# Kernel optimization log

Measured on AMD Instinct MI355X. Metric: run time of the kernel, lower is better.

The kernel has to match this reference:

```python
import jax, jax.numpy as jnp
import numpy as np

SEQ_LEN = 2_097_152  # free sequence dimension
NUM_SYMBOLS = 10
NUM_STATES = 10
NUM_CLASSES = 2


def setup_inputs() -> dict:
    key = jax.random.key(0)
    k1, k2, k3, k4 = jax.random.split(key, 4)
    # x[t] is a probability distribution over symbols (soft one-hot), matching
    # the automaton semantics and keeping the 2M-step recurrence numerically stable.
    x = jax.random.uniform(k1, (SEQ_LEN, NUM_SYMBOLS), dtype=jnp.float32)
    x = x / jnp.sum(x, axis=1, keepdims=True)
    # Parameters, initialized exactly as in the torch module (__init__ softmaxes).
    P = jax.nn.softmax(jax.random.normal(k2, (NUM_SYMBOLS, NUM_STATES, NUM_STATES), dtype=jnp.float32), axis=2)
    start_state = jax.nn.softmax(jax.random.normal(k3, (NUM_STATES,), dtype=jnp.float32), axis=0)
    accept_states = jax.nn.softmax(jax.random.normal(k4, (NUM_STATES, NUM_CLASSES), dtype=jnp.float32), axis=1)
    return {"x": x, "P": P, "start_state": start_state, "accept_states": accept_states}


def reference(x, P, start_state, accept_states):
    # Sequential recurrence: s_{t+1} = s_t @ (sum_k x[t,k] * P[k])
    def step(s, xt):
        Wt = jnp.einsum('k,kij->ij', xt, P)  # [S, S] symbol-weighted transition
        return s @ Wt, None
    s, _ = jax.lax.scan(step, start_state, x)
    return s @ accept_states  # [num_classes]
```

## Files before the change

### kernel.cpp

```cpp
#include <hip/hip_runtime.h>

#define TEN 10

typedef float v2f __attribute__((ext_vector_type(2)));

__global__ __attribute__((amdgpu_flat_work_group_size(256, 256),
                          amdgpu_waves_per_eu(1, 1)))
void automaton_chunks(const float* __restrict__ x, const float* __restrict__ P,
                      float* __restrict__ outBlk, long long T, int C)
{
    __shared__ __align__(16) float lds[8704];

    const int tid  = threadIdx.x;
    const int wave = tid >> 6;
    const int lane = tid & 63;
    const int grp  = lane / 5;
    const int sub  = lane % 5;
    const bool active = (grp < 12);
    const int cib  = wave * 12 + grp;
    const int j0 = 2 * sub, j1 = j0 + 1;

    v2f p2[TEN][TEN];
    v2f m2[2][5];
    long long Lc = 0;
    const float2* xp = nullptr;
    float* slot = lds + (active ? cib : 0) * 132;

    if (active) {
        const long long chunk = (long long)blockIdx.x * 48 + cib;
        const long long s0 = chunk * T / C;
        const long long s1 = (chunk + 1) * T / C;
        Lc = s1 - s0;
        xp = reinterpret_cast<const float2*>(x) + s0 * 5;
#pragma unroll
        for (int k = 0; k < TEN; ++k)
#pragma unroll
            for (int a = 0; a < TEN; ++a) {
                const float2 v = *reinterpret_cast<const float2*>(P + k * 100 + a * TEN + j0);
                p2[k][a].x = v.x;
                p2[k][a].y = v.y;
            }
#pragma unroll
        for (int c = 0; c < 2; ++c)
#pragma unroll
            for (int i = 0; i < 5; ++i) {
                const int jc = 2 * sub + c;
                m2[c][i].x = (2 * i     == jc) ? 1.0f : 0.0f;
                m2[c][i].y = (2 * i + 1 == jc) ? 1.0f : 0.0f;
            }
    }

    float2 nx0, nx1, nx2, nx3, nx4;
    if (active) { nx0 = xp[0]; nx1 = xp[1]; nx2 = xp[2]; nx3 = xp[3]; nx4 = xp[4]; xp += 5; }

    if (active) {
#pragma unroll 1
        for (long long s = 0; s < Lc; ++s) {
            const float xs[TEN] = {nx0.x, nx0.y, nx1.x, nx1.y, nx2.x,
                                   nx2.y, nx3.x, nx3.y, nx4.x, nx4.y};
            v2f xv2[TEN];
#pragma unroll
            for (int k = 0; k < TEN; ++k) { xv2[k].x = xs[k]; xv2[k].y = xs[k]; }
            if (s + 1 < Lc) {
                nx0 = xp[0]; nx1 = xp[1]; nx2 = xp[2]; nx3 = xp[3]; nx4 = xp[4];
                xp += 5;
            }

            {
                float* c0 = slot + j0 * 12;
                reinterpret_cast<float4*>(c0)[0] = make_float4(m2[0][0].x, m2[0][0].y, m2[0][1].x, m2[0][1].y);
                reinterpret_cast<float4*>(c0)[1] = make_float4(m2[0][2].x, m2[0][2].y, m2[0][3].x, m2[0][3].y);
                reinterpret_cast<float2*>(c0 + 8)[0] = make_float2(m2[0][4].x, m2[0][4].y);
                float* c1 = slot + j1 * 12;
                reinterpret_cast<float4*>(c1)[0] = make_float4(m2[1][0].x, m2[1][0].y, m2[1][1].x, m2[1][1].y);
                reinterpret_cast<float4*>(c1)[1] = make_float4(m2[1][2].x, m2[1][2].y, m2[1][3].x, m2[1][3].y);
                reinterpret_cast<float2*>(c1 + 8)[0] = make_float2(m2[1][4].x, m2[1][4].y);
            }
            __builtin_amdgcn_wave_barrier();

            v2f w2[TEN];
#pragma unroll
            for (int a = 0; a < TEN; ++a) {
                v2f acc = xv2[0] * p2[0][a];
#pragma unroll
                for (int k = 1; k < TEN; ++k)
                    acc = __builtin_elementwise_fma(xv2[k], p2[k][a], acc);
                w2[a] = acc;
            }

#pragma unroll
            for (int a = 0; a < TEN; ++a) {
                const float4 v0 = reinterpret_cast<const float4*>(slot + a * 12)[0];
                const float4 v1 = reinterpret_cast<const float4*>(slot + a * 12)[1];
                const float2 v2 = reinterpret_cast<const float2*>(slot + a * 12 + 8)[0];
                v2f cc[5];
                cc[0].x = v0.x; cc[0].y = v0.y;
                cc[1].x = v0.z; cc[1].y = v0.w;
                cc[2].x = v1.x; cc[2].y = v1.y;
                cc[3].x = v1.z; cc[3].y = v1.w;
                cc[4].x = v2.x; cc[4].y = v2.y;
                v2f wb0, wb1;
                wb0.x = w2[a].x; wb0.y = w2[a].x;
                wb1.x = w2[a].y; wb1.y = w2[a].y;
                if (a == 0) {
#pragma unroll
                    for (int i = 0; i < 5; ++i) {
                        m2[0][i] = cc[i] * wb0;
                        m2[1][i] = cc[i] * wb1;
                    }
                } else {
#pragma unroll
                    for (int i = 0; i < 5; ++i) {
                        m2[0][i] = __builtin_elementwise_fma(cc[i], wb0, m2[0][i]);
                        m2[1][i] = __builtin_elementwise_fma(cc[i], wb1, m2[1][i]);
                    }
                }
            }
            __builtin_amdgcn_wave_barrier();
        }
    }

    __syncthreads();
    if (active) {
        float* t = lds + cib * 120;
#pragma unroll
        for (int i = 0; i < 5; ++i) {
            t[(2 * i)     * 12 + j0] = m2[0][i].x;
            t[(2 * i + 1) * 12 + j0] = m2[0][i].y;
            t[(2 * i)     * 12 + j1] = m2[1][i].x;
            t[(2 * i + 1) * 12 + j1] = m2[1][i].y;
        }
    }
    __syncthreads();

    {
        const float* src = lds;
        float* dst = lds + 5760;
        int n = 48;
        while (n > 3) {
            const int np = n >> 1;
            const int pI = tid / TEN;
            const int r  = tid % TEN;
            if (pI < np) {
                const float* A = src + (2 * pI) * 120;
                const float* B = src + (2 * pI + 1) * 120;
                float ar[TEN];
#pragma unroll
                for (int j = 0; j < TEN; ++j) ar[j] = A[r * 12 + j];
                float c[TEN] = {0, 0, 0, 0, 0, 0, 0, 0, 0, 0};
#pragma unroll
                for (int a = 0; a < TEN; ++a) {
                    const float ma = ar[a];
#pragma unroll
                    for (int j = 0; j < TEN; ++j) c[j] = fmaf(ma, B[a * 12 + j], c[j]);
                }
                float* Cp = dst + pI * 120;
#pragma unroll
                for (int j = 0; j < TEN; ++j) Cp[r * 12 + j] = c[j];
            }
            __syncthreads();
            const float* ts = src; src = dst; dst = const_cast<float*>(ts);
            n = np;
        }
        if (tid < TEN) {
            const int r = tid;
            float ar[TEN];
#pragma unroll
            for (int j = 0; j < TEN; ++j) ar[j] = src[r * 12 + j];
            float c[TEN] = {0, 0, 0, 0, 0, 0, 0, 0, 0, 0};
#pragma unroll
            for (int a = 0; a < TEN; ++a) {
                const float ma = ar[a];
#pragma unroll
                for (int j = 0; j < TEN; ++j) c[j] = fmaf(ma, src[120 + a * 12 + j], c[j]);
            }
#pragma unroll
            for (int j = 0; j < TEN; ++j) lds[5760 + r * 12 + j] = c[j];
        }
        __syncthreads();
        if (tid < TEN) {
            const int r = tid;
            float c[TEN] = {0, 0, 0, 0, 0, 0, 0, 0, 0, 0};
#pragma unroll
            for (int a = 0; a < TEN; ++a) {
                const float ma = lds[5760 + r * 12 + a];
#pragma unroll
                for (int j = 0; j < TEN; ++j) c[j] = fmaf(ma, src[240 + a * 12 + j], c[j]);
            }
            float* dr = outBlk + (size_t)blockIdx.x * 100 + r * TEN;
#pragma unroll
            for (int j = 0; j < TEN; ++j) dr[j] = c[j];
        }
    }
}

__device__ __forceinline__ void tree64(float* lds, int tid)
{
    const int q     = tid >> 2;
    const int sub   = tid & 3;
    const int rbase = (sub == 3) ? 8 : sub * 3;
    const int r0 = rbase, r1 = rbase + 1;
    const int r2 = (rbase + 2 > 9) ? 9 : rbase + 2;
    const bool w2 = (sub < 2);

    for (int np = 32; np >= 1; np >>= 1) {
        float c[3][TEN];
        if (q < np) {
            const float* A = lds + (2 * q) * 120;
            const float* B = lds + (2 * q + 1) * 120;
            float ar[3][TEN];
#pragma unroll
            for (int t = 0; t < 3; ++t) {
                const int rt = (t == 0) ? r0 : (t == 1) ? r1 : r2;
                const float4 a0 = reinterpret_cast<const float4*>(A + rt * 12)[0];
                const float4 a1 = reinterpret_cast<const float4*>(A + rt * 12)[1];
                const float2 a2 = reinterpret_cast<const float2*>(A + rt * 12 + 8)[0];
                ar[t][0]=a0.x; ar[t][1]=a0.y; ar[t][2]=a0.z; ar[t][3]=a0.w;
                ar[t][4]=a1.x; ar[t][5]=a1.y; ar[t][6]=a1.z; ar[t][7]=a1.w;
                ar[t][8]=a2.x; ar[t][9]=a2.y;
#pragma unroll
                for (int j = 0; j < TEN; ++j) c[t][j] = 0.0f;
            }
#pragma unroll
            for (int a = 0; a < TEN; ++a) {
                const float4 b0 = reinterpret_cast<const float4*>(B + a * 12)[0];
                const float4 b1 = reinterpret_cast<const float4*>(B + a * 12)[1];
                const float2 b2 = reinterpret_cast<const float2*>(B + a * 12 + 8)[0];
                const float br[TEN] = {b0.x,b0.y,b0.z,b0.w,b1.x,b1.y,b1.z,b1.w,b2.x,b2.y};
#pragma unroll
                for (int t = 0; t < 3; ++t) {
                    const float ma = ar[t][a];
#pragma unroll
                    for (int j = 0; j < TEN; ++j) c[t][j] = fmaf(ma, br[j], c[t][j]);
                }
            }
        }
        __syncthreads();
        if (q < np) {
            float* C = lds + q * 120;
#pragma unroll
            for (int t = 0; t < 3; ++t) {
                const int rt = (t == 0) ? r0 : (t == 1) ? r1 : r2;
                if (t < 2 || w2) {
                    float* cr = C + rt * 12;
                    reinterpret_cast<float4*>(cr)[0] = make_float4(c[t][0], c[t][1], c[t][2], c[t][3]);
                    reinterpret_cast<float4*>(cr)[1] = make_float4(c[t][4], c[t][5], c[t][6], c[t][7]);
                    reinterpret_cast<float2*>(cr + 8)[0] = make_float2(c[t][8], c[t][9]);
                }
            }
        }
        __syncthreads();
    }
}

__global__ void automaton_final(const float* __restrict__ blkM,
                                const float* __restrict__ start,
                                const float* __restrict__ acc,
                                float* __restrict__ outv)
{
    __shared__ __align__(16) float lds[7680];
    __shared__ float sv[TEN];
    const int tid = threadIdx.x;
    const int q   = tid >> 2;
    const int sub = tid & 3;
    const int rbase = (sub == 3) ? 8 : sub * 3;
    const int rr0 = rbase, rr1 = rbase + 1;
    const int rr2 = (rbase + 2 > 9) ? 9 : rbase + 2;
    const bool w2 = (sub < 2);

    float a[3][TEN];
    {
        const int rr[3] = {rr0, rr1, rr2};
        const float* A0 = blkM + (size_t)(4 * q) * 100;
#pragma unroll
        for (int t = 0; t < 3; ++t) {
            const float2* pp = reinterpret_cast<const float2*>(A0 + rr[t] * TEN);
            const float2 a0 = pp[0], a1 = pp[1], a2 = pp[2], a3 = pp[3], a4 = pp[4];
            a[t][0]=a0.x; a[t][1]=a0.y; a[t][2]=a1.x; a[t][3]=a1.y; a[t][4]=a2.x;
            a[t][5]=a2.y; a[t][6]=a3.x; a[t][7]=a3.y; a[t][8]=a4.x; a[t][9]=a4.y;
        }
    }
#pragma unroll 1
    for (int i = 1; i < 4; ++i) {
        const float* B = blkM + (size_t)(4 * q + i) * 100;
        float c[3][TEN];
#pragma unroll
        for (int t = 0; t < 3; ++t)
#pragma unroll
            for (int j = 0; j < TEN; ++j) c[t][j] = 0.0f;
#pragma unroll
        for (int aa = 0; aa < TEN; ++aa) {
            const float2* br = reinterpret_cast<const float2*>(B + aa * TEN);
            const float2 b0 = br[0], b1 = br[1], b2 = br[2], b3 = br[3], b4 = br[4];
            const float bv[TEN] = {b0.x,b0.y,b1.x,b1.y,b2.x,b2.y,b3.x,b3.y,b4.x,b4.y};
#pragma unroll
            for (int t = 0; t < 3; ++t) {
                const float ma = a[t][aa];
#pragma unroll
                for (int j = 0; j < TEN; ++j) c[t][j] = fmaf(ma, bv[j], c[t][j]);
            }
        }
#pragma unroll
        for (int t = 0; t < 3; ++t)
#pragma unroll
            for (int j = 0; j < TEN; ++j) a[t][j] = c[t][j];
    }
    {
        float* dst = lds + q * 120;
#pragma unroll
        for (int t = 0; t < 3; ++t) {
            const int rt = (t == 0) ? rr0 : (t == 1) ? rr1 : rr2;
            if (t < 2 || w2) {
                float* dr = dst + rt * 12;
                reinterpret_cast<float4*>(dr)[0] = make_float4(a[t][0], a[t][1], a[t][2], a[t][3]);
                reinterpret_cast<float4*>(dr)[1] = make_float4(a[t][4], a[t][5], a[t][6], a[t][7]);
                reinterpret_cast<float2*>(dr + 8)[0] = make_float2(a[t][8], a[t][9]);
            }
        }
    }
    __syncthreads();
    tree64(lds, tid);

    if (tid < TEN) {
        const int j = tid;
        float v = 0.0f;
#pragma unroll
        for (int r = 0; r < TEN; ++r) v = fmaf(start[r], lds[r * 12 + j], v);
        sv[j] = v;
    }
    __syncthreads();
    if (tid == 0) {
        float o0 = 0.0f, o1 = 0.0f;
#pragma unroll
        for (int j = 0; j < TEN; ++j) {
            o0 = fmaf(sv[j], acc[2 * j + 0], o0);
            o1 = fmaf(sv[j], acc[2 * j + 1], o1);
        }
        outv[0] = o0;
        outv[1] = o1;
    }
}

extern "C" void kernel_launch(void* const* d_in, const int* in_sizes, int n_in,
                              void* d_out, int out_size, void* d_ws, size_t ws_size,
                              hipStream_t stream)
{
    const float* x     = (const float*)d_in[0];
    const float* P     = (const float*)d_in[1];
    const float* start = (const float*)d_in[2];
    const float* acc   = (const float*)d_in[3];
    float* out         = (float*)d_out;

    const long long T = (long long)in_sizes[0] / TEN;
    const int C = 12288;

    float* blkM = (float*)d_ws;

    automaton_chunks<<<256, 256, 0, stream>>>(x, P, blkM, T, C);
    automaton_final<<<1, 256, 0, stream>>>(blkM, start, acc, out);
}
```

Measured before the change: 267.7 us.

## Double chunk count, allow two waves per EU, use op_sel packed FMA asm

```diff
diff --git a/kernel.cpp b/kernel.cpp
--- a/kernel.cpp
+++ b/kernel.cpp
@@ -4,8 +4,16 @@
 
 typedef float v2f __attribute__((ext_vector_type(2)));
 
+#define PK_MUL_S0LO(d,s0,s1)   asm("v_pk_mul_f32 %0, %1, %2 op_sel:[0,0] op_sel_hi:[0,1]"         : "=v"(d)  : "v"(s0), "v"(s1))
+#define PK_FMA_S0LO(acc,s0,s1) asm("v_pk_fma_f32 %0, %1, %2, %0 op_sel:[0,0,0] op_sel_hi:[0,1,1]" : "+v"(acc) : "v"(s0), "v"(s1))
+#define PK_FMA_S0HI(acc,s0,s1) asm("v_pk_fma_f32 %0, %1, %2, %0 op_sel:[1,0,0] op_sel_hi:[1,1,1]" : "+v"(acc) : "v"(s0), "v"(s1))
+#define PK_MUL_S1LO(d,s0,s1)   asm("v_pk_mul_f32 %0, %1, %2 op_sel:[0,0] op_sel_hi:[1,0]"         : "=v"(d)  : "v"(s0), "v"(s1))
+#define PK_MUL_S1HI(d,s0,s1)   asm("v_pk_mul_f32 %0, %1, %2 op_sel:[0,1] op_sel_hi:[1,1]"         : "=v"(d)  : "v"(s0), "v"(s1))
+#define PK_FMA_S1LO(acc,s0,s1) asm("v_pk_fma_f32 %0, %1, %2, %0 op_sel:[0,0,0] op_sel_hi:[1,0,1]" : "+v"(acc) : "v"(s0), "v"(s1))
+#define PK_FMA_S1HI(acc,s0,s1) asm("v_pk_fma_f32 %0, %1, %2, %0 op_sel:[0,1,0] op_sel_hi:[1,1,1]" : "+v"(acc) : "v"(s0), "v"(s1))
+
 __global__ __attribute__((amdgpu_flat_work_group_size(256, 256),
-                          amdgpu_waves_per_eu(1, 1)))
+                          amdgpu_waves_per_eu(2, 2)))
 void automaton_chunks(const float* __restrict__ x, const float* __restrict__ P,
                       float* __restrict__ outBlk, long long T, int C)
 {
@@ -22,16 +30,17 @@
 
     v2f p2[TEN][TEN];
     v2f m2[2][5];
-    long long Lc = 0;
-    const float2* xp = nullptr;
+    int Lc = 0;
+    const v2f* xp = nullptr;
     float* slot = lds + (active ? cib : 0) * 132;
+    float* wb0  = slot + j0 * 12;
 
     if (active) {
         const long long chunk = (long long)blockIdx.x * 48 + cib;
         const long long s0 = chunk * T / C;
         const long long s1 = (chunk + 1) * T / C;
-        Lc = s1 - s0;
-        xp = reinterpret_cast<const float2*>(x) + s0 * 5;
+        Lc = (int)(s1 - s0);
+        xp = reinterpret_cast<const v2f*>(x) + s0 * 5;
 #pragma unroll
         for (int k = 0; k < TEN; ++k)
 #pragma unroll
@@ -50,72 +59,72 @@
             }
     }
 
-    float2 nx0, nx1, nx2, nx3, nx4;
-    if (active) { nx0 = xp[0]; nx1 = xp[1]; nx2 = xp[2]; nx3 = xp[3]; nx4 = xp[4]; xp += 5; }
+    v2f nxv0, nxv1, nxv2, nxv3, nxv4;
+    if (active) {
+        nxv0 = xp[0]; nxv1 = xp[1]; nxv2 = xp[2]; nxv3 = xp[3]; nxv4 = xp[4];
+        xp += 5;
+    }
 
     if (active) {
 #pragma unroll 1
-        for (long long s = 0; s < Lc; ++s) {
-            const float xs[TEN] = {nx0.x, nx0.y, nx1.x, nx1.y, nx2.x,
-                                   nx2.y, nx3.x, nx3.y, nx4.x, nx4.y};
-            v2f xv2[TEN];
-#pragma unroll
-            for (int k = 0; k < TEN; ++k) { xv2[k].x = xs[k]; xv2[k].y = xs[k]; }
+        for (int s = 0; s < Lc; ++s) {
+            {
+                *reinterpret_cast<v2f*>(wb0 + 0)  = m2[0][0];
+                *reinterpret_cast<v2f*>(wb0 + 2)  = m2[0][1];
+                *reinterpret_cast<v2f*>(wb0 + 4)  = m2[0][2];
+                *reinterpret_cast<v2f*>(wb0 + 6)  = m2[0][3];
+                *reinterpret_cast<v2f*>(wb0 + 8)  = m2[0][4];
+                *reinterpret_cast<v2f*>(wb0 + 12) = m2[1][0];
+                *reinterpret_cast<v2f*>(wb0 + 14) = m2[1][1];
+                *reinterpret_cast<v2f*>(wb0 + 16) = m2[1][2];
+                *reinterpret_cast<v2f*>(wb0 + 18) = m2[1][3];
+                *reinterpret_cast<v2f*>(wb0 + 20) = m2[1][4];
+            }
+            __builtin_amdgcn_wave_barrier();
+
+            v2f px0, px1, px2, px3, px4;
             if (s + 1 < Lc) {
-                nx0 = xp[0]; nx1 = xp[1]; nx2 = xp[2]; nx3 = xp[3]; nx4 = xp[4];
+                px0 = xp[0]; px1 = xp[1]; px2 = xp[2]; px3 = xp[3]; px4 = xp[4];
                 xp += 5;
             }
 
-            {
-                float* c0 = slot + j0 * 12;
-                reinterpret_cast<float4*>(c0)[0] = make_float4(m2[0][0].x, m2[0][0].y, m2[0][1].x, m2[0][1].y);
-                reinterpret_cast<float4*>(c0)[1] = make_float4(m2[0][2].x, m2[0][2].y, m2[0][3].x, m2[0][3].y);
-                reinterpret_cast<float2*>(c0 + 8)[0] = make_float2(m2[0][4].x, m2[0][4].y);
-                float* c1 = slot + j1 * 12;
-                reinterpret_cast<float4*>(c1)[0] = make_float4(m2[1][0].x, m2[1][0].y, m2[1][1].x, m2[1][1].y);
-                reinterpret_cast<float4*>(c1)[1] = make_float4(m2[1][2].x, m2[1][2].y, m2[1][3].x, m2[1][3].y);
-                reinterpret_cast<float2*>(c1 + 8)[0] = make_float2(m2[1][4].x, m2[1][4].y);
-            }
-            __builtin_amdgcn_wave_barrier();
-
-            v2f w2[TEN];
-#pragma unroll
-            for (int a = 0; a < TEN; ++a) {
-                v2f acc = xv2[0] * p2[0][a];
-#pragma unroll
-                for (int k = 1; k < TEN; ++k)
-                    acc = __builtin_elementwise_fma(xv2[k], p2[k][a], acc);
-                w2[a] = acc;
-            }
-
-#pragma unroll
-            for (int a = 0; a < TEN; ++a) {
-                const float4 v0 = reinterpret_cast<const float4*>(slot + a * 12)[0];
-                const float4 v1 = reinterpret_cast<const float4*>(slot + a * 12)[1];
-                const float2 v2 = reinterpret_cast<const float2*>(slot + a * 12 + 8)[0];
-                v2f cc[5];
-                cc[0].x = v0.x; cc[0].y = v0.y;
-                cc[1].x = v0.z; cc[1].y = v0.w;
-                cc[2].x = v1.x; cc[2].y = v1.y;
-                cc[3].x = v1.z; cc[3].y = v1.w;
-                cc[4].x = v2.x; cc[4].y = v2.y;
-                v2f wb0, wb1;
-                wb0.x = w2[a].x; wb0.y = w2[a].x;
-                wb1.x = w2[a].y; wb1.y = w2[a].y;
+#pragma unroll
+            for (int a = 0; a < TEN; ++a) {
+                union { float4 q; v2f h[2]; } u0, u1;
+                union { float2 f; v2f v;   } u2;
+                u0.q = *reinterpret_cast<const float4*>(slot + a * 12);
+                u1.q = *reinterpret_cast<const float4*>(slot + a * 12 + 4);
+                u2.f = *reinterpret_cast<const float2*>(slot + a * 12 + 8);
+                const v2f c0 = u0.h[0], c1 = u0.h[1], c2 = u1.h[0], c3 = u1.h[1], c4 = u2.v;
+
+                v2f w;
+                PK_MUL_S0LO(w, nxv0, p2[0][a]);
+                PK_FMA_S0HI(w, nxv0, p2[1][a]);
+                PK_FMA_S0LO(w, nxv1, p2[2][a]);
+                PK_FMA_S0HI(w, nxv1, p2[3][a]);
+                PK_FMA_S0LO(w, nxv2, p2[4][a]);
+                PK_FMA_S0HI(w, nxv2, p2[5][a]);
+                PK_FMA_S0LO(w, nxv3, p2[6][a]);
+                PK_FMA_S0HI(w, nxv3, p2[7][a]);
+                PK_FMA_S0LO(w, nxv4, p2[8][a]);
+                PK_FMA_S0HI(w, nxv4, p2[9][a]);
+
                 if (a == 0) {
-#pragma unroll
-                    for (int i = 0; i < 5; ++i) {
-                        m2[0][i] = cc[i] * wb0;
-                        m2[1][i] = cc[i] * wb1;
-                    }
+                    PK_MUL_S1LO(m2[0][0], c0, w);  PK_MUL_S1HI(m2[1][0], c0, w);
+                    PK_MUL_S1LO(m2[0][1], c1, w);  PK_MUL_S1HI(m2[1][1], c1, w);
+                    PK_MUL_S1LO(m2[0][2], c2, w);  PK_MUL_S1HI(m2[1][2], c2, w);
+                    PK_MUL_S1LO(m2[0][3], c3, w);  PK_MUL_S1HI(m2[1][3], c3, w);
+                    PK_MUL_S1LO(m2[0][4], c4, w);  PK_MUL_S1HI(m2[1][4], c4, w);
                 } else {
-#pragma unroll
-                    for (int i = 0; i < 5; ++i) {
-                        m2[0][i] = __builtin_elementwise_fma(cc[i], wb0, m2[0][i]);
-                        m2[1][i] = __builtin_elementwise_fma(cc[i], wb1, m2[1][i]);
-                    }
+                    PK_FMA_S1LO(m2[0][0], c0, w);  PK_FMA_S1HI(m2[1][0], c0, w);
+                    PK_FMA_S1LO(m2[0][1], c1, w);  PK_FMA_S1HI(m2[1][1], c1, w);
+                    PK_FMA_S1LO(m2[0][2], c2, w);  PK_FMA_S1HI(m2[1][2], c2, w);
+                    PK_FMA_S1LO(m2[0][3], c3, w);  PK_FMA_S1HI(m2[1][3], c3, w);
+                    PK_FMA_S1LO(m2[0][4], c4, w);  PK_FMA_S1HI(m2[1][4], c4, w);
                 }
             }
+
+            nxv0 = px0; nxv1 = px1; nxv2 = px2; nxv3 = px3; nxv4 = px4;
             __builtin_amdgcn_wave_barrier();
         }
     }
@@ -271,7 +280,7 @@
     float a[3][TEN];
     {
         const int rr[3] = {rr0, rr1, rr2};
-        const float* A0 = blkM + (size_t)(4 * q) * 100;
+        const float* A0 = blkM + (size_t)(8 * q) * 100;
 #pragma unroll
         for (int t = 0; t < 3; ++t) {
             const float2* pp = reinterpret_cast<const float2*>(A0 + rr[t] * TEN);
@@ -281,8 +290,8 @@
         }
     }
 #pragma unroll 1
-    for (int i = 1; i < 4; ++i) {
-        const float* B = blkM + (size_t)(4 * q + i) * 100;
+    for (int i = 1; i < 8; ++i) {
+        const float* B = blkM + (size_t)(8 * q + i) * 100;
         float c[3][TEN];
 #pragma unroll
         for (int t = 0; t < 3; ++t)
@@ -352,10 +361,10 @@
     float* out         = (float*)d_out;
 
     const long long T = (long long)in_sizes[0] / TEN;
-    const int C = 12288;
+    const int C = 24576;
 
     float* blkM = (float*)d_ws;
 
-    automaton_chunks<<<256, 256, 0, stream>>>(x, P, blkM, T, C);
+    automaton_chunks<<<512, 256, 0, stream>>>(x, P, blkM, T, C);
     automaton_final<<<1, 256, 0, stream>>>(blkM, start, acc, out);
 }
```

After: 272.3 us. No clear change (+1.7%).
